# Kernel tuning notes

Measured on AMD Instinct MI355X. Metric: run time of the kernel, lower is better.

The kernel has to match this reference:

```python
import jax, jax.numpy as jnp
import numpy as np

B, S, I, H, O, L = 64, 1024, 512, 512, 512, 3


def setup_inputs() -> dict:
    key = jax.random.key(0)
    ks = jax.random.split(key, 14)
    sc = 0.05  # small init to avoid gate saturation
    inp = {
        "input": jax.random.normal(ks[0], (B, S, I), jnp.float32),
        "hidden_state": jax.random.normal(ks[1], (B, L, H), jnp.float32),
        # gate params; x-side Linear has bias, h-side has none (as in torch module)
        "Wzx": jax.random.normal(ks[2], (L, I, H), jnp.float32) * sc,
        "bzx": jnp.zeros((L, H), jnp.float32),
        "Wzh": jax.random.normal(ks[3], (L, H, H), jnp.float32) * sc,
        "Wrx": jax.random.normal(ks[4], (L, I, H), jnp.float32) * sc,
        "brx": jnp.zeros((L, H), jnp.float32),
        "Wrh": jax.random.normal(ks[5], (L, H, H), jnp.float32) * sc,
        "Wgx": jax.random.normal(ks[6], (L, I, H), jnp.float32) * sc,
        "bgx": jnp.zeros((L, H), jnp.float32),
        "Wgh": jax.random.normal(ks[7], (L, H, H), jnp.float32) * sc,
        "Wout": jax.random.normal(ks[8], (H, O), jnp.float32) * sc,
        "bout": jnp.zeros((O,), jnp.float32),
    }
    return inp


def reference(input, hidden_state, Wzx, bzx, Wzh, Wrx, brx, Wrh, Wgx, bgx, Wgh, Wout, bout):
    n_layers = Wzx.shape[0]
    Bn = input.shape[0]
    Hn = hidden_state.shape[2]
    # layer_states: n_layers initial states + one extra zeros slot (matches torch code)
    states0 = jnp.concatenate(
        [jnp.transpose(hidden_state, (1, 0, 2)),
         jnp.zeros((1, Bn, Hn), input.dtype)], axis=0)  # (L+1, B, H)

    def step(states, x_t):
        x = x_t  # (B, I)
        for l in range(n_layers):
            # NOTE: faithfully reproduces the original's indexing: layer l reads
            # states[l], which for l>=1 was just overwritten by layer l-1 this step.
            h = states[l]
            z = jax.nn.sigmoid(x @ Wzx[l] + bzx[l] + h @ Wzh[l])
            r = jax.nn.sigmoid(x @ Wrx[l] + brx[l] + h @ Wrh[l])
            g = jnp.tanh(x @ Wgx[l] + bgx[l] + (r * h) @ Wgh[l])
            h = z * h + (1.0 - z) * g
            x = h  # dropout=0 -> identity
            states = states.at[l + 1].set(h)
        out_t = x @ Wout + bout  # (B, O)
        return states, out_t

    states_f, outs = jax.lax.scan(step, states0, jnp.transpose(input, (1, 0, 2)))
    layer_output = jnp.transpose(outs, (1, 0, 2))          # (B, S, O)
    hidden_out = jnp.transpose(states_f[:n_layers], (1, 0, 2))  # (B, L, H)
    return layer_output, hidden_out
```

## Files before the change

### kernel.cpp

```cpp
#include <hip/hip_runtime.h>


typedef __attribute__((ext_vector_type(4))) float f32x4;
typedef __attribute__((ext_vector_type(8))) __bf16 bf16x8;

#define NROWS 65536
#define HID_OFF 33554432ull

__device__ __forceinline__ void gload16(const void* g, void* l) {
  __builtin_amdgcn_global_load_lds((const __attribute__((address_space(1))) void*)g,
                                   (__attribute__((address_space(3))) void*)l,
                                   16, 0, 0);
}
__device__ __forceinline__ float sigmoidf_(float x) { return 1.f / (1.f + __expf(-x)); }
__device__ __forceinline__ float tanh_fast(float x) {
  const float e = __expf(2.f * x);
  return 1.f - 2.f / (e + 1.f);
}

__device__ __forceinline__ void stage32(const __bf16* __restrict__ src, int k0,
                                        __bf16* lds, int w, int lane) {
#pragma unroll
  for (int i = 0; i < 2; ++i) {
    const int s0 = (w * 2 + i) * 64;
    const int s = s0 + lane;
    const int row = s >> 2;
    const int cc = ((s & 3) ^ (row >> 1)) & 3;
    gload16(src + (size_t)row * 512 + k0 + cc * 8, lds + s0 * 8);
  }
}

__device__ __forceinline__ bf16x8 frag32(const __bf16* t, int row, int lane) {
  const int c = (((lane >> 4) ^ (row >> 1)) & 3);
  return *(const bf16x8*)(t + row * 32 + c * 8);
}

__device__ __forceinline__ void stage_ht(const __bf16* __restrict__ src,
                                         __bf16* Ht, int w, int lane) {
#pragma unroll
  for (int i = 0; i < 8; ++i) {
    const int s0 = i * 256 + w * 64;
    const int s = s0 + lane;
    const int row = s >> 4, cc = s & 15;
    gload16(src + (size_t)row * 512 + cc * 8, Ht + s0 * 8);
  }
  asm volatile("s_waitcnt vmcnt(0)");
  __builtin_amdgcn_sched_barrier(0);
  __builtin_amdgcn_s_barrier();
  __builtin_amdgcn_sched_barrier(0);
}

template<int EPI, bool L0>
__global__ __launch_bounds__(256, 3) void gemm9(
    const __bf16* __restrict__ A,
    const __bf16* __restrict__ Bt,
    int tiles_n, int row_off,
    const float* __restrict__ bias,
    const float* __restrict__ cterm,
    const float* __restrict__ h0f,
    const __bf16* __restrict__ haux,
    const __bf16* __restrict__ zf,
    const __bf16* __restrict__ gf,
    __bf16* __restrict__ o_rh,
    __bf16* __restrict__ o_h,
    float* __restrict__ o_f)
{
  __shared__ alignas(16) __bf16 smem[24576];
  __bf16* const A0 = smem;
  __bf16* const B0 = smem + 4096;
  __bf16* const A1 = smem + 8192;
  __bf16* const B1 = smem + 12288;
  __bf16* const A2 = smem + 16384;
  __bf16* const B2 = smem + 20480;

  const int tid = threadIdx.x, lane = tid & 63, w = tid >> 6;

  int bid = blockIdx.x;
  {
    const int nwg = gridDim.x;
    const int q = nwg >> 3, r = nwg & 7;
    const int x = bid & 7, rest = bid >> 3;
    bid = (x < r ? x * (q + 1) : r * (q + 1) + (x - r) * q) + rest;
  }
  const int tm = bid / tiles_n;
  const int tn = bid - tm * tiles_n;
  const size_t arow0 = (size_t)tm * 128;
  const int brow0 = tn * 128;
  const __bf16* const Ab = A + arow0 * 512;
  const __bf16* const Bb = Bt + (size_t)brow0 * 512;

  const int wr = (w >> 1) * 64;
  const int wc = (w & 1) * 64;

  f32x4 acc[4][4];
  const f32x4 zz = {0.f, 0.f, 0.f, 0.f};
#pragma unroll
  for (int i = 0; i < 4; ++i)
#pragma unroll
    for (int j = 0; j < 4; ++j) acc[i][j] = zz;

  auto stepf = [&](int t, const __bf16* cA, const __bf16* cB,
                   __bf16* nA, __bf16* nB, int vm) {
    if (nA) {
      stage32(Ab, (t + 2) * 32, nA, w, lane);
      stage32(Bb, (t + 2) * 32, nB, w, lane);
    }
    bf16x8 af[4], bb4[4];
#pragma unroll
    for (int i = 0; i < 4; ++i) {
      af[i]  = frag32(cA, wr + i * 16 + (lane & 15), lane);
      bb4[i] = frag32(cB, wc + i * 16 + (lane & 15), lane);
    }
#pragma unroll
    for (int mi = 0; mi < 4; ++mi)
#pragma unroll
      for (int ni = 0; ni < 4; ++ni)
        acc[mi][ni] = __builtin_amdgcn_mfma_f32_16x16x32_bf16(af[mi], bb4[ni], acc[mi][ni], 0, 0, 0);
    if (vm == 4) {
      asm volatile("s_waitcnt vmcnt(4)");
      __builtin_amdgcn_sched_barrier(0);
    } else if (vm == 0) {
      asm volatile("s_waitcnt vmcnt(0)");
      __builtin_amdgcn_sched_barrier(0);
    }
    __builtin_amdgcn_s_barrier();
    __builtin_amdgcn_sched_barrier(0);
  };

  stage32(Ab, 0, A0, w, lane);
  stage32(Bb, 0, B0, w, lane);
  stage32(Ab, 32, A1, w, lane);
  stage32(Bb, 32, B1, w, lane);
  asm volatile("s_waitcnt vmcnt(4)");
  __builtin_amdgcn_sched_barrier(0);
  __builtin_amdgcn_s_barrier();
  __builtin_amdgcn_sched_barrier(0);

#pragma unroll 1
  for (int it = 0; it < 4; ++it) {
    const int t = it * 3;
    stepf(t,     A0, B0, A2, B2, 4);
    stepf(t + 1, A1, B1, A0, B0, 4);
    stepf(t + 2, A2, B2, A1, B1, 4);
  }
  stepf(12, A0, B0, A2, B2, 4);
  stepf(13, A1, B1, A0, B0, 4);
  stepf(14, A2, B2, nullptr, nullptr, 0);
  stepf(15, A0, B0, nullptr, nullptr, -1);

  const int fcol = lane & 15;
  const int frow = (lane >> 4) * 4;
  const int bb0 = (row_off + (int)arow0) >> 10;

  if (EPI == 0) {
    if (tn < 4) {
      const size_t foff = ((size_t)(tm * 4 + tn)) * 16384 + (size_t)tid * 64;
      __bf16* zw = (__bf16*)zf;
#pragma unroll
      for (int mi = 0; mi < 4; ++mi) {
        bf16x8 p0, p1;
#pragma unroll
        for (int ni = 0; ni < 4; ++ni)
#pragma unroll
          for (int j = 0; j < 4; ++j) {
            const int gcol = brow0 + wc + ni * 16 + fcol;
            float c = acc[mi][ni][j] + bias[gcol];
            if (L0) c += cterm[bb0 * 1024 + gcol];
            const float v = sigmoidf_(c);
            const int idx = ni * 4 + j;
            if (idx < 8) p0[idx] = (__bf16)v; else p1[idx - 8] = (__bf16)v;
          }
        *(bf16x8*)(zw + foff + mi * 16) = p0;
        *(bf16x8*)(zw + foff + mi * 16 + 8) = p1;
      }
    } else if (tn < 8) {
      if (!L0) stage_ht(haux + arow0 * 512 + (tn - 4) * 128, smem, w, lane);
#pragma unroll
      for (int mi = 0; mi < 4; ++mi)
#pragma unroll
        for (int ni = 0; ni < 4; ++ni)
#pragma unroll
          for (int j = 0; j < 4; ++j) {
            const int rloc = (int)arow0 + wr + mi * 16 + frow + j;
            const int gcol = brow0 + wc + ni * 16 + fcol;
            const int nn = gcol - 512;
            float c = acc[mi][ni][j] + bias[gcol];
            if (L0) c += cterm[bb0 * 1024 + gcol];
            const float rv = sigmoidf_(c);
            const float h = L0 ? h0f[bb0 * 1536 + nn]
                               : (float)smem[(wr + mi * 16 + frow + j) * 128 + wc + ni * 16 + fcol];
            o_rh[(size_t)rloc * 512 + nn] = (__bf16)(rv * h);
          }
    } else {
      const size_t foff = ((size_t)(tm * 4 + (tn - 8))) * 16384 + (size_t)tid * 64;
      __bf16* gw = (__bf16*)gf;
#pragma unroll
      for (int mi = 0; mi < 4; ++mi) {
        bf16x8 p0, p1;
#pragma unroll
        for (int ni = 0; ni < 4; ++ni)
#pragma unroll
          for (int j = 0; j < 4; ++j) {
            const int gcol = brow0 + wc + ni * 16 + fcol;
            const float v = acc[mi][ni][j] + bias[gcol];
            const int idx = ni * 4 + j;
            if (idx < 8) p0[idx] = (__bf16)v; else p1[idx - 8] = (__bf16)v;
          }
        *(bf16x8*)(gw + foff + mi * 16) = p0;
        *(bf16x8*)(gw + foff + mi * 16 + 8) = p1;
      }
    }
  } else if (EPI == 1) {
    const size_t foff = ((size_t)(tm * 4 + tn)) * 16384 + (size_t)tid * 64;
    bf16x8 zr[4][2], gr[4][2];
#pragma unroll
    for (int mi = 0; mi < 4; ++mi) {
      zr[mi][0] = *(const bf16x8*)(zf + foff + mi * 16);
      zr[mi][1] = *(const bf16x8*)(zf + foff + mi * 16 + 8);
      gr[mi][0] = *(const bf16x8*)(gf + foff + mi * 16);
      gr[mi][1] = *(const bf16x8*)(gf + foff + mi * 16 + 8);
    }
    if (!L0) stage_ht(haux + arow0 * 512 + tn * 128, smem, w, lane);
    const bool has_last = (o_f != nullptr) && ((tm & 7) == 7);
#pragma unroll
    for (int mi = 0; mi < 4; ++mi) {
#pragma unroll
      for (int ni = 0; ni < 4; ++ni)
#pragma unroll
        for (int j = 0; j < 4; ++j) {
          const int rloc = (int)arow0 + wr + mi * 16 + frow + j;
          const int gcol = brow0 + wc + ni * 16 + fcol;
          const int idx = ni * 4 + j;
          const float zv = (float)(idx < 8 ? zr[mi][0][idx] : zr[mi][1][idx - 8]);
          const float gp = (float)(idx < 8 ? gr[mi][0][idx] : gr[mi][1][idx - 8]);
          const float gv = tanh_fast(gp + acc[mi][ni][j]);
          const float h = L0 ? h0f[bb0 * 1536 + gcol]
                             : (float)smem[(wr + mi * 16 + frow + j) * 128 + wc + ni * 16 + fcol];
          const float hv = zv * h + (1.f - zv) * gv;
          o_h[(size_t)rloc * 512 + gcol] = (__bf16)hv;
          if (has_last && ((rloc & 1023) == 1023))
            o_f[(size_t)bb0 * 1536 + gcol] = (float)(__bf16)hv;
        }
    }
  } else {
#pragma unroll
    for (int mi = 0; mi < 4; ++mi)
#pragma unroll
      for (int ni = 0; ni < 4; ++ni)
#pragma unroll
        for (int j = 0; j < 4; ++j) {
          const int rloc = (int)arow0 + wr + mi * 16 + frow + j;
          const int gcol = brow0 + wc + ni * 16 + fcol;
          o_f[(size_t)rloc * 512 + gcol] = acc[mi][ni][j] + bias[gcol];
        }
  }
}


__global__ void prep_pack(const float* __restrict__ Wzx, const float* __restrict__ Wzh,
                          const float* __restrict__ Wrx, const float* __restrict__ Wrh,
                          const float* __restrict__ Wgx, const float* __restrict__ Wgh,
                          const float* __restrict__ Wout,
                          __bf16* __restrict__ W1t, __bf16* __restrict__ Wght,
                          __bf16* __restrict__ Woutt)
{
  const int slot = blockIdx.z;
  const float* srcA;
  const float* srcB = nullptr;
  __bf16* dst;
  if (slot < 9) {
    const int l = slot / 3, g = slot % 3;
    srcA = (g == 0 ? Wzx : g == 1 ? Wrx : Wgx) + (size_t)l * 512 * 512;
    if (l > 0 && g < 2) srcB = (g == 0 ? Wzh : Wrh) + (size_t)l * 512 * 512;
    dst = W1t + (size_t)l * 1536 * 512 + (size_t)g * 512 * 512;
  } else if (slot < 12) {
    const int l = slot - 9;
    srcA = Wgh + (size_t)l * 512 * 512;
    dst = Wght + (size_t)l * 512 * 512;
  } else {
    srcA = Wout;
    dst = Woutt;
  }
  __shared__ float tile[32][33];
  const int k0 = blockIdx.x * 32;
  const int n0 = blockIdx.y * 32;
  const int tx = threadIdx.x;
  const int ty = threadIdx.y;
  for (int i = ty; i < 32; i += 8) {
    float v = srcA[(size_t)(k0 + i) * 512 + n0 + tx];
    if (srcB) v += srcB[(size_t)(k0 + i) * 512 + n0 + tx];
    tile[i][tx] = v;
  }
  __syncthreads();
  for (int i = ty; i < 32; i += 8)
    dst[(size_t)(n0 + i) * 512 + k0 + tx] = (__bf16)tile[tx][i];
}

__global__ void cterm_kernel(const float* __restrict__ hidden,
                             const float* __restrict__ Wzh,
                             const float* __restrict__ Wrh,
                             float* __restrict__ Cterm)
{
  const int idx = blockIdx.x * blockDim.x + threadIdx.x;
  const int b = idx >> 10;
  const int n = idx & 1023;
  const float* W = (n < 512 ? Wzh : Wrh);
  const int nn = n & 511;
  const float* h0 = hidden + (size_t)b * 1536;
  float acc = 0.f;
  for (int k = 0; k < 512; ++k) acc += h0[k] * W[(size_t)k * 512 + nn];
  Cterm[idx] = acc;
}

__global__ void small_prep(const float* __restrict__ bzx, const float* __restrict__ brx,
                           const float* __restrict__ bgx, const float* __restrict__ hidden,
                           float* __restrict__ bias1, float* __restrict__ out_hidden)
{
  const int idx = blockIdx.x * blockDim.x + threadIdx.x;
  if (idx < 3 * 1536) {
    const int l = idx / 1536, j = idx % 1536;
    const float* src = (j < 512 ? bzx : j < 1024 ? brx : bgx);
    bias1[idx] = src[l * 512 + (j & 511)];
  }
  const int hidx = idx - 3 * 1536;
  if (hidx >= 0 && hidx < 64 * 512) {
    const int b = hidx >> 9, n = hidx & 511;
    out_hidden[(size_t)b * 1536 + n] = hidden[(size_t)b * 1536 + n];
  }
}

__global__ void convert_x(const float* __restrict__ src, __bf16* __restrict__ dst, long n)
{
  const long i = ((long)blockIdx.x * blockDim.x + threadIdx.x) * 8;
  if (i >= n) return;
  const f32x4 a = *(const f32x4*)(src + i);
  const f32x4 b = *(const f32x4*)(src + i + 4);
  bf16x8 o;
  o[0] = (__bf16)a[0]; o[1] = (__bf16)a[1]; o[2] = (__bf16)a[2]; o[3] = (__bf16)a[3];
  o[4] = (__bf16)b[0]; o[5] = (__bf16)b[1]; o[6] = (__bf16)b[2]; o[7] = (__bf16)b[3];
  *(bf16x8*)(dst + i) = o;
}

extern "C" void kernel_launch(void* const* d_in, const int* in_sizes, int n_in,
                              void* d_out, int out_size, void* d_ws, size_t ws_size,
                              hipStream_t stream) {
  const float* input  = (const float*)d_in[0];
  const float* hidden = (const float*)d_in[1];
  const float* Wzx = (const float*)d_in[2];
  const float* bzx = (const float*)d_in[3];
  const float* Wzh = (const float*)d_in[4];
  const float* Wrx = (const float*)d_in[5];
  const float* brx = (const float*)d_in[6];
  const float* Wrh = (const float*)d_in[7];
  const float* Wgx = (const float*)d_in[8];
  const float* bgx = (const float*)d_in[9];
  const float* Wgh = (const float*)d_in[10];
  const float* Wout = (const float*)d_in[11];
  const float* bout = (const float*)d_in[12];

  float* out = (float*)d_out;
  float* out_hidden = out + HID_OFF;

  char* ws = (char*)d_ws;
  size_t off = 0;
  auto carve = [&](size_t bytes) -> void* {
    off = (off + 255) & ~(size_t)255;
    void* p = ws + off;
    off += bytes;
    return p;
  };

  __bf16* W1t   = (__bf16*)carve(3ull * 1536 * 512 * 2);
  __bf16* Wght  = (__bf16*)carve(3ull * 512 * 512 * 2);
  __bf16* Woutt = (__bf16*)carve(512ull * 512 * 2);
  float*  bias1 = (float*) carve(3ull * 1536 * 4);
  float*  Cterm = (float*) carve(64ull * 1024 * 4);
  const size_t fixed_end = off;

  long chunk_rows = NROWS;
  int C = 1;
  while (C < 32) {
    const size_t need = ((fixed_end + 255) & ~(size_t)255) +
                        5ull * (size_t)chunk_rows * 512 * 2 + 5 * 256;
    if (need <= ws_size) break;
    C *= 2;
    chunk_rows /= 2;
  }
  __bf16* bufA  = (__bf16*)carve((size_t)chunk_rows * 512 * 2);
  __bf16* bufB  = (__bf16*)carve((size_t)chunk_rows * 512 * 2);
  __bf16* zfrag = (__bf16*)carve((size_t)chunk_rows * 512 * 2);
  __bf16* rhb   = (__bf16*)carve((size_t)chunk_rows * 512 * 2);
  __bf16* gfrag = (__bf16*)carve((size_t)chunk_rows * 512 * 2);

  small_prep<<<(3 * 1536 + 64 * 512 + 255) / 256, 256, 0, stream>>>(
      bzx, brx, bgx, hidden, bias1, out_hidden);
  dim3 tp_grid(16, 16, 13), tp_blk(32, 8);
  prep_pack<<<tp_grid, tp_blk, 0, stream>>>(Wzx, Wzh, Wrx, Wrh, Wgx, Wgh, Wout,
                                            W1t, Wght, Woutt);
  cterm_kernel<<<65536 / 256, 256, 0, stream>>>(hidden, Wzh, Wrh, Cterm);

  for (int c = 0; c < C; ++c) {
    const long row_off = (long)c * chunk_rows;
    const long nelem = chunk_rows * 512;
    const int mt = (int)(chunk_rows / 128);

    convert_x<<<(int)((nelem / 8 + 255) / 256), 256, 0, stream>>>(
        input + (size_t)row_off * 512, bufA, nelem);

    gemm9<0, true><<<mt * 12, 256, 0, stream>>>(
        bufA, W1t, 12, (int)row_off, bias1, Cterm, hidden, nullptr,
        zfrag, gfrag, rhb, nullptr, nullptr);
    gemm9<1, true><<<mt * 4, 256, 0, stream>>>(
        rhb, Wght, 4, (int)row_off, nullptr, nullptr, hidden, nullptr,
        zfrag, gfrag, nullptr, bufB, out_hidden + 512);

    gemm9<0, false><<<mt * 12, 256, 0, stream>>>(
        bufB, W1t + 1536 * 512, 12, (int)row_off, bias1 + 1536, nullptr, nullptr, bufB,
        zfrag, gfrag, rhb, nullptr, nullptr);
    gemm9<1, false><<<mt * 4, 256, 0, stream>>>(
        rhb, Wght + 512 * 512, 4, (int)row_off, nullptr, nullptr, nullptr, bufB,
        zfrag, gfrag, nullptr, bufA, out_hidden + 1024);

    gemm9<0, false><<<mt * 12, 256, 0, stream>>>(
        bufA, W1t + 2 * 1536 * 512, 12, (int)row_off, bias1 + 3072, nullptr, nullptr, bufA,
        zfrag, gfrag, rhb, nullptr, nullptr);
    gemm9<1, false><<<mt * 4, 256, 0, stream>>>(
        rhb, Wght + 2 * 512 * 512, 4, (int)row_off, nullptr, nullptr, nullptr, bufA,
        zfrag, gfrag, nullptr, bufB, nullptr);

    gemm9<2, false><<<mt * 4, 256, 0, stream>>>(
        bufB, Woutt, 4, (int)row_off, bout, nullptr, nullptr, nullptr,
        nullptr, nullptr, nullptr, nullptr, out + (size_t)row_off * 512);
  }
}
```

Before: 863.1 us.

## Deepen GEMM pipeline to four LDS stages with register double-buffered fragments

The GEMM kernel moves from a three-stage to a four-stage LDS ring, prefetching three K-slices ahead. It also double-buffers the MFMA operand fragments in registers, so the LDS reads for the next step are issued while the current step's MFMAs run. The aim is to hide global-load and LDS-read latency behind matrix math. In exchange, LDS use grows to 64KB and register pressure rises, and launch bounds drop from 3 to 2 workgroups per CU, which lowers occupancy.

```diff
diff --git a/kernel.cpp b/kernel.cpp
--- a/kernel.cpp
+++ b/kernel.cpp
@@ -51,7 +51,7 @@
 }
 
 template<int EPI, bool L0>
-__global__ __launch_bounds__(256, 3) void gemm9(
+__global__ __launch_bounds__(256, 2) void gemm11(
     const __bf16* __restrict__ A,
     const __bf16* __restrict__ Bt,
     int tiles_n, int row_off,
@@ -65,13 +65,15 @@
     __bf16* __restrict__ o_h,
     float* __restrict__ o_f)
 {
-  __shared__ alignas(16) __bf16 smem[24576];
+  __shared__ alignas(16) __bf16 smem[32768];
   __bf16* const A0 = smem;
   __bf16* const B0 = smem + 4096;
   __bf16* const A1 = smem + 8192;
   __bf16* const B1 = smem + 12288;
   __bf16* const A2 = smem + 16384;
   __bf16* const B2 = smem + 20480;
+  __bf16* const A3 = smem + 24576;
+  __bf16* const B3 = smem + 28672;
 
   const int tid = threadIdx.x, lane = tid & 63, w = tid >> 6;
 
@@ -99,23 +101,34 @@
 #pragma unroll
     for (int j = 0; j < 4; ++j) acc[i][j] = zz;
 
-  auto stepf = [&](int t, const __bf16* cA, const __bf16* cB,
-                   __bf16* nA, __bf16* nB, int vm) {
-    if (nA) {
-      stage32(Ab, (t + 2) * 32, nA, w, lane);
-      stage32(Bb, (t + 2) * 32, nB, w, lane);
-    }
-    bf16x8 af[4], bb4[4];
+  bf16x8 fA0[4], fB0[4], fA1[4], fB1[4];
+
+  auto rdfrag = [&](const __bf16* TA, const __bf16* TB,
+                    bf16x8 (&fa)[4], bf16x8 (&fb)[4]) {
 #pragma unroll
     for (int i = 0; i < 4; ++i) {
-      af[i]  = frag32(cA, wr + i * 16 + (lane & 15), lane);
-      bb4[i] = frag32(cB, wc + i * 16 + (lane & 15), lane);
-    }
+      fa[i] = frag32(TA, wr + i * 16 + (lane & 15), lane);
+      fb[i] = frag32(TB, wc + i * 16 + (lane & 15), lane);
+    }
+  };
+  auto domfma = [&](bf16x8 (&fa)[4], bf16x8 (&fb)[4]) {
 #pragma unroll
     for (int mi = 0; mi < 4; ++mi)
 #pragma unroll
       for (int ni = 0; ni < 4; ++ni)
-        acc[mi][ni] = __builtin_amdgcn_mfma_f32_16x16x32_bf16(af[mi], bb4[ni], acc[mi][ni], 0, 0, 0);
+        acc[mi][ni] = __builtin_amdgcn_mfma_f32_16x16x32_bf16(fa[mi], fb[ni], acc[mi][ni], 0, 0, 0);
+  };
+
+  auto stepp = [&](int kst, __bf16* sA, __bf16* sB,
+                   const __bf16* rA, const __bf16* rB,
+                   bf16x8 (&fna)[4], bf16x8 (&fnb)[4],
+                   bf16x8 (&fca)[4], bf16x8 (&fcb)[4], int vm) {
+    if (sA) {
+      stage32(Ab, kst, sA, w, lane);
+      stage32(Bb, kst, sB, w, lane);
+    }
+    if (rA) rdfrag(rA, rB, fna, fnb);
+    domfma(fca, fcb);
     if (vm == 4) {
       asm volatile("s_waitcnt vmcnt(4)");
       __builtin_amdgcn_sched_barrier(0);
@@ -131,22 +144,27 @@
   stage32(Bb, 0, B0, w, lane);
   stage32(Ab, 32, A1, w, lane);
   stage32(Bb, 32, B1, w, lane);
+  stage32(Ab, 64, A2, w, lane);
+  stage32(Bb, 64, B2, w, lane);
   asm volatile("s_waitcnt vmcnt(4)");
   __builtin_amdgcn_sched_barrier(0);
   __builtin_amdgcn_s_barrier();
   __builtin_amdgcn_sched_barrier(0);
+  rdfrag(A0, B0, fA0, fB0);
 
 #pragma unroll 1
-  for (int it = 0; it < 4; ++it) {
-    const int t = it * 3;
-    stepf(t,     A0, B0, A2, B2, 4);
-    stepf(t + 1, A1, B1, A0, B0, 4);
-    stepf(t + 2, A2, B2, A1, B1, 4);
-  }
-  stepf(12, A0, B0, A2, B2, 4);
-  stepf(13, A1, B1, A0, B0, 4);
-  stepf(14, A2, B2, nullptr, nullptr, 0);
-  stepf(15, A0, B0, nullptr, nullptr, -1);
+  for (int it = 0; it < 3; ++it) {
+    const int kb = it * 128;
+    stepp(kb +  96, A3, B3, A1, B1, fA1, fB1, fA0, fB0, 4);
+    stepp(kb + 128, A0, B0, A2, B2, fA0, fB0, fA1, fB1, 4);
+    stepp(kb + 160, A1, B1, A3, B3, fA1, fB1, fA0, fB0, 4);
+    stepp(kb + 192, A2, B2, A0, B0, fA0, fB0, fA1, fB1, 4);
+  }
+  stepp(480, A3, B3, A1, B1, fA1, fB1, fA0, fB0, 4);
+  stepp(0, nullptr, nullptr, A2, B2, fA0, fB0, fA1, fB1, 0);
+  stepp(0, nullptr, nullptr, A3, B3, fA1, fB1, fA0, fB0, -1);
+  domfma(fA1, fB1);
+  __builtin_amdgcn_s_barrier();
 
   const int fcol = lane & 15;
   const int frow = (lane >> 4) * 4;
@@ -407,28 +425,28 @@
     convert_x<<<(int)((nelem / 8 + 255) / 256), 256, 0, stream>>>(
         input + (size_t)row_off * 512, bufA, nelem);
 
-    gemm9<0, true><<<mt * 12, 256, 0, stream>>>(
+    gemm11<0, true><<<mt * 12, 256, 0, stream>>>(
         bufA, W1t, 12, (int)row_off, bias1, Cterm, hidden, nullptr,
         zfrag, gfrag, rhb, nullptr, nullptr);
-    gemm9<1, true><<<mt * 4, 256, 0, stream>>>(
+    gemm11<1, true><<<mt * 4, 256, 0, stream>>>(
         rhb, Wght, 4, (int)row_off, nullptr, nullptr, hidden, nullptr,
         zfrag, gfrag, nullptr, bufB, out_hidden + 512);
 
-    gemm9<0, false><<<mt * 12, 256, 0, stream>>>(
+    gemm11<0, false><<<mt * 12, 256, 0, stream>>>(
         bufB, W1t + 1536 * 512, 12, (int)row_off, bias1 + 1536, nullptr, nullptr, bufB,
         zfrag, gfrag, rhb, nullptr, nullptr);
-    gemm9<1, false><<<mt * 4, 256, 0, stream>>>(
+    gemm11<1, false><<<mt * 4, 256, 0, stream>>>(
         rhb, Wght + 512 * 512, 4, (int)row_off, nullptr, nullptr, nullptr, bufB,
         zfrag, gfrag, nullptr, bufA, out_hidden + 1024);
 
-    gemm9<0, false><<<mt * 12, 256, 0, stream>>>(
+    gemm11<0, false><<<mt * 12, 256, 0, stream>>>(
         bufA, W1t + 2 * 1536 * 512, 12, (int)row_off, bias1 + 3072, nullptr, nullptr, bufA,
         zfrag, gfrag, rhb, nullptr, nullptr);
-    gemm9<1, false><<<mt * 4, 256, 0, stream>>>(
+    gemm11<1, false><<<mt * 4, 256, 0, stream>>>(
         rhb, Wght + 2 * 512 * 512, 4, (int)row_off, nullptr, nullptr, nullptr, bufA,
         zfrag, gfrag, nullptr, bufB, nullptr);
 
-    gemm9<2, false><<<mt * 4, 256, 0, stream>>>(
+    gemm11<2, false><<<mt * 4, 256, 0, stream>>>(
         bufB, Woutt, 4, (int)row_off, bout, nullptr, nullptr, nullptr,
         nullptr, nullptr, nullptr, nullptr, out + (size_t)row_off * 512);
   }
```

Measured after the change: 925.0 us. 1.07x slower.
